# Kernel tuning notes

Hardware: AMD Instinct MI355X
Metric: run time of the kernel (lower is better)

The kernel has to match this reference:

```python
import jax, jax.numpy as jnp
import numpy as np

B, N, M, D = 64, 512, 1024, 128

def setup_inputs() -> dict:
    key = jax.random.key(0)
    ks = jax.random.split(key, 7)
    s = 1.0 / np.sqrt(D)
    return {
        "h_c": jax.random.normal(ks[0], (B, N, D), dtype=jnp.float32),
        "h_p": jax.random.normal(ks[1], (B, M, D), dtype=jnp.float32),
        "U_w": jax.random.normal(ks[2], (D, D), dtype=jnp.float32) * s,
        "U_b": jax.random.normal(ks[3], (D,), dtype=jnp.float32) * s,
        "V_w": jax.random.normal(ks[4], (D, D), dtype=jnp.float32) * s,
        "V_b": jax.random.normal(ks[5], (D,), dtype=jnp.float32) * s,
        "q": jax.random.normal(ks[6], (D,), dtype=jnp.float32),
    }

def reference(h_c, h_p, U_w, U_b, V_w, V_b, q):
    # ReLU-activated linear projections (torch Linear: x @ W.T + b)
    Uc = jax.nn.relu(jnp.einsum('bnd,ed->bne', h_c, U_w) + U_b)  # (B,N,D)
    Vp = jax.nn.relu(jnp.einsum('bmd,ed->bme', h_p, V_w) + V_b)  # (B,M,D)
    # bilinear attention scores and softmax over protein axis
    attn = jnp.einsum('bnd,bmd->bnm', Uc, Vp)                    # (B,N,M)
    weights = jax.nn.softmax(attn, axis=-1)
    context = jnp.einsum('bnm,bmd->bnd', weights, Vp)            # (B,N,D)
    joint = (Uc + context) * q                                   # (B,N,D)
    return joint.mean(axis=1)                                    # (B,D)
```

## Files before the change

kernel.cpp:

```cpp
#include <hip/hip_runtime.h>
#include <hip/hip_bf16.h>
#include <cstdint>

#define BB 64
#define NN 512
#define MM 1024
#define DD 128

typedef __bf16 bf16x8 __attribute__((ext_vector_type(8)));
typedef float f32x4 __attribute__((ext_vector_type(4)));

static __device__ __forceinline__ unsigned short f2bf(float f) {
    union { float f; unsigned int i; } v; v.f = f;
    unsigned int x = v.i;
    x += 0x7FFFu + ((x >> 16) & 1u);
    return (unsigned short)(x >> 16);
}
static __device__ __forceinline__ unsigned int f2bf2(float a, float b) {
    union { __hip_bfloat162 h; unsigned int u; } c;
    c.h = __float22bfloat162_rn(make_float2(a, b));
    return c.u;
}
static __device__ __forceinline__ void async16(const void* g, void* l) {
    __builtin_amdgcn_global_load_lds(
        (const __attribute__((address_space(1))) void*)g,
        (__attribute__((address_space(3))) void*)l, 16, 0, 0);
}

__global__ __launch_bounds__(256) void wcvt_kernel(
    const float* __restrict__ Wu, const float* __restrict__ Wv,
    unsigned short* __restrict__ out)
{
    const float* W = blockIdx.x ? Wv : Wu;
    unsigned short* o = out + blockIdx.x * 16384;
    const float s = blockIdx.x ? 1.0f : 1.44269504088896f;
    #pragma unroll
    for (int i = 0; i < 8; ++i) {
        int ch = i * 256 + threadIdx.x;
        int r = ch >> 4, c = ch & 15;
        const float4* src = (const float4*)(W + r * 128 + c * 8);
        float4 a = src[0], b = src[1];
        uint4 v = { f2bf2(a.x * s, a.y * s), f2bf2(a.z * s, a.w * s),
                    f2bf2(b.x * s, b.y * s), f2bf2(b.z * s, b.w * s) };
        *(uint4*)&o[r * 128 + ((c ^ (r & 7)) << 3)] = v;
    }
}

__global__ __launch_bounds__(256, 4) void proj_kernel(
    const float* __restrict__ hp,
    const float* __restrict__ hc,
    const unsigned short* __restrict__ Wcv,
    const float* __restrict__ Ub,
    const float* __restrict__ Vb,
    unsigned short* __restrict__ Y,
    unsigned short* __restrict__ YT,
    unsigned short* __restrict__ Ucg,
    float* __restrict__ colsum)
{
    __shared__ __align__(16) unsigned short Ws[17408];
    unsigned short* Ys = Ws;
    unsigned short* Ts = Ws + 8192;
    const int t = threadIdx.x;
    const int lane = t & 63;
    const int wave = t >> 6;
    const int n16 = lane & 15, q = lane >> 4;
    const bool isC = blockIdx.x >= (BB * MM / 64);
    const float LOG2E = 1.44269504088896f;

    const long row0 = isC ? (long)(blockIdx.x - BB * MM / 64) * 64
                          : (long)blockIdx.x * 64;
    const float* X = isC ? hc : hp;
    const unsigned short* Wb = isC ? Wcv : (Wcv + 16384);
    const float* bias = isC ? Ub : Vb;

    float4 xv[8];
    {
        const float* xrow = X + (row0 + wave * 16 + n16) * DD + q * 8;
        #pragma unroll
        for (int kk = 0; kk < 4; ++kk) {
            xv[2 * kk]     = *(const float4*)(xrow + kk * 32);
            xv[2 * kk + 1] = *(const float4*)(xrow + kk * 32 + 4);
        }
    }
    #pragma unroll
    for (int i = 0; i < 8; ++i)
        async16(Wb + (wave * 512 + i * 64 + lane) * 8, Ws + wave * 4096 + i * 512);
    __syncthreads();

    f32x4 acc[8];
    #pragma unroll
    for (int j = 0; j < 8; ++j) acc[j] = {0.f, 0.f, 0.f, 0.f};

    #pragma unroll
    for (int kk = 0; kk < 4; ++kk) {
        float4 x0 = xv[2 * kk], x1 = xv[2 * kk + 1];
        union { bf16x8 v; unsigned int u[4]; } a;
        a.u[0] = f2bf2(x0.x, x0.y); a.u[1] = f2bf2(x0.z, x0.w);
        a.u[2] = f2bf2(x1.x, x1.y); a.u[3] = f2bf2(x1.z, x1.w);
        #pragma unroll
        for (int j = 0; j < 8; ++j) {
            bf16x8 b = *(const bf16x8*)&Ws[(j * 16 + n16) * 128
                                           + (((q + 4 * kk) ^ (n16 & 7)) << 3)];
            acc[j] = __builtin_amdgcn_mfma_f32_16x16x32_bf16(a.v, b, acc[j], 0, 0, 0);
        }
    }

    unsigned short yb[8][4];
    float colp[8];
    #pragma unroll
    for (int j = 0; j < 8; ++j) {
        const float bv = isC ? bias[j * 16 + n16] * LOG2E : bias[j * 16 + n16];
        float y[4], s = 0.f;
        #pragma unroll
        for (int r = 0; r < 4; ++r) {
            float v = acc[j][r] + bv;
            v = v > 0.f ? v : 0.f;
            y[r] = v;
            s += v;
        }
        colp[j] = s;
        uint2 u = { f2bf2(y[0], y[1]), f2bf2(y[2], y[3]) };
        *(uint2*)&yb[j][0] = u;
    }
    __syncthreads();

    if (!isC) {
        #pragma unroll
        for (int j = 0; j < 8; ++j) {
            const int e = j * 16 + n16;
            #pragma unroll
            for (int r = 0; r < 4; ++r)
                Ys[(wave * 16 + q * 4 + r) * 128 + e] = yb[j][r];
            *(uint2*)&Ts[e * 72 + wave * 16 + q * 4] = *(uint2*)&yb[j][0];
        }
        __syncthreads();
        uint4* dstY = (uint4*)(Y + row0 * DD);
        const long b = row0 >> 10;
        const long mt = (row0 & 1023) >> 6;
        uint4* dstT = (uint4*)(YT + ((b * 16 + mt) * 128) * 64);
        #pragma unroll
        for (int i = 0; i < 4; ++i) {
            int idx = i * 256 + t;
            dstY[idx] = ((const uint4*)Ys)[idx];
            int e = idx >> 3, m = (idx & 7) * 8;
            dstT[idx] = *(const uint4*)&Ts[e * 72 + m];
        }
    } else {
        #pragma unroll
        for (int j = 0; j < 8; ++j) {
            colp[j] += __shfl_xor(colp[j], 16);
            colp[j] += __shfl_xor(colp[j], 32);
        }
        float* cs = (float*)Ts;
        if (q == 0) {
            #pragma unroll
            for (int j = 0; j < 8; ++j)
                cs[wave * 128 + j * 16 + n16] = colp[j];
        }
        #pragma unroll
        for (int j = 0; j < 8; ++j) {
            const int e = j * 16 + n16;
            #pragma unroll
            for (int r = 0; r < 4; ++r)
                Ys[(wave * 16 + q * 4 + r) * 128 + e] = yb[j][r];
        }
        __syncthreads();
        const int c = (int)(row0 >> 6);
        uint4* dstU = (uint4*)(Ucg + row0 * DD);
        #pragma unroll
        for (int i = 0; i < 4; ++i) {
            int idx = i * 256 + t;
            dstU[idx] = ((const uint4*)Ys)[idx];
        }
        if (t < 128)
            colsum[(long)c * DD + t] = cs[t] + cs[128 + t] + cs[256 + t] + cs[384 + t];
    }
}

static __device__ __forceinline__ void attn_iter(
    int mt, unsigned short* bD, const unsigned short* bR, unsigned short* Ps,
    const unsigned short* __restrict__ vpb,
    const unsigned short* __restrict__ vtb,
    int wave, int lane, int n16, int q, int a_off,
    const bf16x8 (&Bg)[4][4],
    bf16x8 (&aC)[4], bf16x8 (&aN)[4],
    f32x4 (&O)[8], float (&lpart)[4])
{
    const int nx = (mt + 1 > 15) ? 15 : mt + 1;
    {
        const unsigned short* st = vtb + nx * 8192;
        unsigned short* dst = bD + wave * 2048;
        #pragma unroll
        for (int i = 0; i < 4; ++i) {
            int L = wave * 256 + i * 64 + lane;
            int r = L >> 3, sc = L & 7, c = sc ^ (r & 7);
            async16(st + r * 64 + c * 8, dst + i * 512);
        }
    }
    __builtin_amdgcn_sched_barrier(0);
    {
        const unsigned short* pa = vpb + nx * 8192 + a_off;
        #pragma unroll
        for (int kk = 0; kk < 4; ++kk)
            aN[kk] = *(const bf16x8*)(pa + kk * 32);
    }

    f32x4 S[4];
    #pragma unroll
    for (int j = 0; j < 4; ++j) S[j] = {0.f, 0.f, 0.f, 0.f};
    __builtin_amdgcn_s_setprio(1);
    #pragma unroll
    for (int kk = 0; kk < 4; ++kk) {
        #pragma unroll
        for (int j = 0; j < 4; ++j)
            S[j] = __builtin_amdgcn_mfma_f32_16x16x32_bf16(aC[kk], Bg[j][kk], S[j], 0, 0, 0);
    }
    __builtin_amdgcn_s_setprio(0);

    #pragma unroll
    for (int j = 0; j < 4; ++j) {
        float p0 = __builtin_exp2f(S[j][0]);
        float p1 = __builtin_exp2f(S[j][1]);
        float p2 = __builtin_exp2f(S[j][2]);
        float p3 = __builtin_exp2f(S[j][3]);
        lpart[j] += (p0 + p1) + (p2 + p3);
        uint2 u = { f2bf2(p0, p1), f2bf2(p2, p3) };
        *(uint2*)&Ps[(j * 16 + n16) * 72 + wave * 16 + q * 4] = u;
    }
    asm volatile("s_waitcnt vmcnt(8) lgkmcnt(0)" ::: "memory");
    __builtin_amdgcn_s_barrier();
    __builtin_amdgcn_sched_barrier(0);

    __builtin_amdgcn_s_setprio(1);
    #pragma unroll
    for (int kk = 0; kk < 2; ++kk) {
        bf16x8 a = *(const bf16x8*)&Ps[(wave * 16 + n16) * 72 + kk * 32 + q * 8];
        #pragma unroll
        for (int j = 0; j < 8; ++j) {
            bf16x8 bb = *(const bf16x8*)&bR[(j * 16 + n16) * 64 + ((kk * 4 + q) ^ (n16 & 7)) * 8];
            O[j] = __builtin_amdgcn_mfma_f32_16x16x32_bf16(a, bb, O[j], 0, 0, 0);
        }
    }
    __builtin_amdgcn_s_setprio(0);
}

__global__ __launch_bounds__(256, 2) void attn_kernel(
    const unsigned short* __restrict__ Ucg,
    const unsigned short* __restrict__ Vp,
    const unsigned short* __restrict__ VpT,
    float* __restrict__ part)
{
    __shared__ __align__(16) unsigned short smem[33792];
    unsigned short* Ps0 = smem + 24576;
    unsigned short* Ps1 = smem + 29184;

    const int t = threadIdx.x;
    const int lane = t & 63;
    const int wave = t >> 6;
    const int n16 = lane & 15, q = lane >> 4;

    const int id = blockIdx.x;
    const int xcd = id & 7;
    const int slot = id >> 3;
    const int b = xcd * 8 + (slot >> 3);
    const int nt = slot & 7;

    const unsigned short* vpb = Vp + (long)b * MM * DD;
    const unsigned short* vtb = VpT + (long)b * MM * DD;
    const unsigned short* ucb = Ucg + ((long)b * NN + nt * 64) * DD;

    bf16x8 Bg[4][4];
    #pragma unroll
    for (int j = 0; j < 4; ++j)
        #pragma unroll
        for (int kk = 0; kk < 4; ++kk)
            Bg[j][kk] = *(const bf16x8*)&ucb[(j * 16 + n16) * 128 + kk * 32 + q * 8];

    const int a_off = (wave * 16 + n16) * 128 + q * 8;
    bf16x8 aA[4], aB[4];
    #pragma unroll
    for (int kk = 0; kk < 4; ++kk)
        aA[kk] = *(const bf16x8*)&vpb[a_off + kk * 32];
    {
        unsigned short* dst = smem + wave * 2048;
        #pragma unroll
        for (int i = 0; i < 4; ++i) {
            int L = wave * 256 + i * 64 + lane;
            int r = L >> 3, sc = L & 7, c = sc ^ (r & 7);
            async16(vtb + r * 64 + c * 8, dst + i * 512);
        }
    }
    asm volatile("s_waitcnt vmcnt(0) lgkmcnt(0)" ::: "memory");
    __builtin_amdgcn_s_barrier();
    __builtin_amdgcn_sched_barrier(0);

    f32x4 O[8];
    #pragma unroll
    for (int j = 0; j < 8; ++j) O[j] = {0.f, 0.f, 0.f, 0.f};
    float lpart[4] = {0.f, 0.f, 0.f, 0.f};

    unsigned short* bR = smem;
    unsigned short* bD = smem + 8192;
    unsigned short* bT = smem + 16384;
    #pragma unroll 1
    for (int mt = 0; mt < 16; mt += 2) {
        attn_iter(mt, bD, bR, Ps0, vpb, vtb, wave, lane, n16, q, a_off, Bg, aA, aB, O, lpart);
        unsigned short* tp = bR; bR = bD; bD = bT; bT = tp;
        attn_iter(mt + 1, bD, bR, Ps1, vpb, vtb, wave, lane, n16, q, a_off, Bg, aB, aA, O, lpart);
        tp = bR; bR = bD; bD = bT; bT = tp;
    }

    #pragma unroll
    for (int j = 0; j < 4; ++j) {
        lpart[j] += __shfl_xor(lpart[j], 16);
        lpart[j] += __shfl_xor(lpart[j], 32);
    }
    float* lred = (float*)Ps0;
    float* red  = lred + 256;
    if (q == 0) {
        #pragma unroll
        for (int j = 0; j < 4; ++j)
            lred[wave * 64 + j * 16 + n16] = lpart[j];
    }
    __syncthreads();

    float inv[4];
    #pragma unroll
    for (int r = 0; r < 4; ++r) {
        int n = wave * 16 + q * 4 + r;
        inv[r] = 1.0f / (lred[n] + lred[64 + n] + lred[128 + n] + lred[192 + n]);
    }

    #pragma unroll
    for (int j = 0; j < 8; ++j) {
        float s = O[j][0] * inv[0] + O[j][1] * inv[1]
                + O[j][2] * inv[2] + O[j][3] * inv[3];
        s += __shfl_xor(s, 16);
        s += __shfl_xor(s, 32);
        if (q == 0)
            red[wave * 128 + j * 16 + n16] = s;
    }
    __syncthreads();
    if (t < 128) {
        float tot = red[t] + red[128 + t] + red[256 + t] + red[384 + t];
        part[(long)(b * 8 + nt) * DD + t] = tot;
    }
}

__global__ __launch_bounds__(256) void finalize_kernel(
    const float* __restrict__ part, const float* __restrict__ colsum,
    const float* __restrict__ qv, float* __restrict__ out)
{
    int i = blockIdx.x * 256 + threadIdx.x;
    int b = i >> 7, d = i & 127;
    const float* p  = part   + (long)b * 8 * DD + d;
    const float* cs = colsum + (long)b * 8 * DD + d;
    float s = 0.f, u = 0.f;
    #pragma unroll
    for (int nt = 0; nt < 8; ++nt) { s += p[nt * DD]; u += cs[nt * DD]; }
    out[i] = (s + u * 0.69314718055994531f) * qv[d] * (1.0f / (float)NN);
}

extern "C" void kernel_launch(void* const* d_in, const int* in_sizes, int n_in,
                              void* d_out, int out_size, void* d_ws, size_t ws_size,
                              hipStream_t stream) {
    const float* h_c = (const float*)d_in[0];
    const float* h_p = (const float*)d_in[1];
    const float* U_w = (const float*)d_in[2];
    const float* U_b = (const float*)d_in[3];
    const float* V_w = (const float*)d_in[4];
    const float* V_b = (const float*)d_in[5];
    const float* qv  = (const float*)d_in[6];
    float* out = (float*)d_out;

    unsigned short* Vp  = (unsigned short*)d_ws;
    unsigned short* VpT = Vp + (size_t)BB * MM * DD;
    unsigned short* Ucg = VpT + (size_t)BB * MM * DD;
    float* part   = (float*)(Ucg + (size_t)BB * NN * DD);
    float* colsum = part + (size_t)BB * 8 * DD;
    unsigned short* Wcv = (unsigned short*)(colsum + (size_t)BB * 8 * DD);

    wcvt_kernel<<<2, 256, 0, stream>>>(U_w, V_w, Wcv);
    proj_kernel<<<BB * MM / 64 + BB * NN / 64, 256, 0, stream>>>(
        h_p, h_c, Wcv, U_b, V_b, Vp, VpT, Ucg, colsum);
    attn_kernel<<<512, 256, 0, stream>>>(Ucg, Vp, VpT, part);
    finalize_kernel<<<32, 256, 0, stream>>>(part, colsum, qv, out);
}
```

Measured before the change: 141.7 us.

## Fuse weight conversion into projection and software-pipeline attention score computation

The separate weight-to-bf16 conversion kernel is removed. Each projection block now loads the fp32 weights, scales and converts them itself, and stores them into a padded (stride 136) LDS layout in place of the XOR swizzle. In the attention kernel the loop is restructured so that scores and exp for tile mt+1 are computed while the PV matmul of tile mt runs. This uses double-buffered P tiles, a two-tile-ahead V^T prefetch and a prologue that handles the first tile. Dropping the kernel launch saves launch overhead, but every projection block now redoes the weight conversion and loads twice as many bytes of weights.

```diff
diff --git a/kernel.cpp b/kernel.cpp
--- a/kernel.cpp
+++ b/kernel.cpp
@@ -27,29 +27,11 @@
         (__attribute__((address_space(3))) void*)l, 16, 0, 0);
 }
 
-__global__ __launch_bounds__(256) void wcvt_kernel(
-    const float* __restrict__ Wu, const float* __restrict__ Wv,
-    unsigned short* __restrict__ out)
-{
-    const float* W = blockIdx.x ? Wv : Wu;
-    unsigned short* o = out + blockIdx.x * 16384;
-    const float s = blockIdx.x ? 1.0f : 1.44269504088896f;
-    #pragma unroll
-    for (int i = 0; i < 8; ++i) {
-        int ch = i * 256 + threadIdx.x;
-        int r = ch >> 4, c = ch & 15;
-        const float4* src = (const float4*)(W + r * 128 + c * 8);
-        float4 a = src[0], b = src[1];
-        uint4 v = { f2bf2(a.x * s, a.y * s), f2bf2(a.z * s, a.w * s),
-                    f2bf2(b.x * s, b.y * s), f2bf2(b.z * s, b.w * s) };
-        *(uint4*)&o[r * 128 + ((c ^ (r & 7)) << 3)] = v;
-    }
-}
-
 __global__ __launch_bounds__(256, 4) void proj_kernel(
     const float* __restrict__ hp,
     const float* __restrict__ hc,
-    const unsigned short* __restrict__ Wcv,
+    const float* __restrict__ Wu,
+    const float* __restrict__ Wv,
     const float* __restrict__ Ub,
     const float* __restrict__ Vb,
     unsigned short* __restrict__ Y,
@@ -57,7 +39,7 @@
     unsigned short* __restrict__ Ucg,
     float* __restrict__ colsum)
 {
-    __shared__ __align__(16) unsigned short Ws[17408];
+    __shared__ __align__(16) unsigned short Ws[128 * 136];
     unsigned short* Ys = Ws;
     unsigned short* Ts = Ws + 8192;
     const int t = threadIdx.x;
@@ -65,12 +47,12 @@
     const int wave = t >> 6;
     const int n16 = lane & 15, q = lane >> 4;
     const bool isC = blockIdx.x >= (BB * MM / 64);
-    const float LOG2E = 1.44269504088896f;
+    const float ws = isC ? 1.44269504088896f : 1.0f;
 
     const long row0 = isC ? (long)(blockIdx.x - BB * MM / 64) * 64
                           : (long)blockIdx.x * 64;
     const float* X = isC ? hc : hp;
-    const unsigned short* Wb = isC ? Wcv : (Wcv + 16384);
+    const float* Wf = isC ? Wu : Wv;
     const float* bias = isC ? Ub : Vb;
 
     float4 xv[8];
@@ -82,9 +64,17 @@
             xv[2 * kk + 1] = *(const float4*)(xrow + kk * 32 + 4);
         }
     }
-    #pragma unroll
-    for (int i = 0; i < 8; ++i)
-        async16(Wb + (wave * 512 + i * 64 + lane) * 8, Ws + wave * 4096 + i * 512);
+    {
+        const float4* Wg = (const float4*)Wf;
+        #pragma unroll
+        for (int i = 0; i < 16; ++i) {
+            int idx = i * 256 + t;
+            float4 v = Wg[idx];
+            int off = idx * 4;
+            uint2 u = { f2bf2(v.x * ws, v.y * ws), f2bf2(v.z * ws, v.w * ws) };
+            *(uint2*)&Ws[(off >> 7) * 136 + (off & 127)] = u;
+        }
+    }
     __syncthreads();
 
     f32x4 acc[8];
@@ -99,8 +89,7 @@
         a.u[2] = f2bf2(x1.x, x1.y); a.u[3] = f2bf2(x1.z, x1.w);
         #pragma unroll
         for (int j = 0; j < 8; ++j) {
-            bf16x8 b = *(const bf16x8*)&Ws[(j * 16 + n16) * 128
-                                           + (((q + 4 * kk) ^ (n16 & 7)) << 3)];
+            bf16x8 b = *(const bf16x8*)&Ws[(j * 16 + n16) * 136 + q * 8 + kk * 32];
             acc[j] = __builtin_amdgcn_mfma_f32_16x16x32_bf16(a.v, b, acc[j], 0, 0, 0);
         }
     }
@@ -109,7 +98,7 @@
     float colp[8];
     #pragma unroll
     for (int j = 0; j < 8; ++j) {
-        const float bv = isC ? bias[j * 16 + n16] * LOG2E : bias[j * 16 + n16];
+        const float bv = bias[j * 16 + n16] * ws;
         float y[4], s = 0.f;
         #pragma unroll
         for (int r = 0; r < 4; ++r) {
@@ -178,7 +167,8 @@
 }
 
 static __device__ __forceinline__ void attn_iter(
-    int mt, unsigned short* bD, const unsigned short* bR, unsigned short* Ps,
+    int mt, unsigned short* bD, const unsigned short* bR,
+    unsigned short* PsW, const unsigned short* PsR,
     const unsigned short* __restrict__ vpb,
     const unsigned short* __restrict__ vtb,
     int wave, int lane, int n16, int q, int a_off,
@@ -186,7 +176,7 @@
     bf16x8 (&aC)[4], bf16x8 (&aN)[4],
     f32x4 (&O)[8], float (&lpart)[4])
 {
-    const int nx = (mt + 1 > 15) ? 15 : mt + 1;
+    const int nx = (mt + 2 > 15) ? 15 : mt + 2;
     {
         const unsigned short* st = vtb + nx * 8192;
         unsigned short* dst = bD + wave * 2048;
@@ -204,37 +194,37 @@
         for (int kk = 0; kk < 4; ++kk)
             aN[kk] = *(const bf16x8*)(pa + kk * 32);
     }
-
-    f32x4 S[4];
-    #pragma unroll
-    for (int j = 0; j < 4; ++j) S[j] = {0.f, 0.f, 0.f, 0.f};
+    asm volatile("s_waitcnt vmcnt(8)" ::: "memory");
+    __builtin_amdgcn_sched_barrier(0);
+
+    if (mt < 15) {
+        f32x4 S[4];
+        #pragma unroll
+        for (int j = 0; j < 4; ++j) S[j] = {0.f, 0.f, 0.f, 0.f};
+        __builtin_amdgcn_s_setprio(1);
+        #pragma unroll
+        for (int kk = 0; kk < 4; ++kk) {
+            #pragma unroll
+            for (int j = 0; j < 4; ++j)
+                S[j] = __builtin_amdgcn_mfma_f32_16x16x32_bf16(aC[kk], Bg[j][kk], S[j], 0, 0, 0);
+        }
+        __builtin_amdgcn_s_setprio(0);
+        #pragma unroll
+        for (int j = 0; j < 4; ++j) {
+            float p0 = __builtin_exp2f(S[j][0]);
+            float p1 = __builtin_exp2f(S[j][1]);
+            float p2 = __builtin_exp2f(S[j][2]);
+            float p3 = __builtin_exp2f(S[j][3]);
+            lpart[j] += (p0 + p1) + (p2 + p3);
+            uint2 u = { f2bf2(p0, p1), f2bf2(p2, p3) };
+            *(uint2*)&PsW[(j * 16 + n16) * 72 + wave * 16 + q * 4] = u;
+        }
+    }
+
     __builtin_amdgcn_s_setprio(1);
     #pragma unroll
-    for (int kk = 0; kk < 4; ++kk) {
-        #pragma unroll
-        for (int j = 0; j < 4; ++j)
-            S[j] = __builtin_amdgcn_mfma_f32_16x16x32_bf16(aC[kk], Bg[j][kk], S[j], 0, 0, 0);
-    }
-    __builtin_amdgcn_s_setprio(0);
-
-    #pragma unroll
-    for (int j = 0; j < 4; ++j) {
-        float p0 = __builtin_exp2f(S[j][0]);
-        float p1 = __builtin_exp2f(S[j][1]);
-        float p2 = __builtin_exp2f(S[j][2]);
-        float p3 = __builtin_exp2f(S[j][3]);
-        lpart[j] += (p0 + p1) + (p2 + p3);
-        uint2 u = { f2bf2(p0, p1), f2bf2(p2, p3) };
-        *(uint2*)&Ps[(j * 16 + n16) * 72 + wave * 16 + q * 4] = u;
-    }
-    asm volatile("s_waitcnt vmcnt(8) lgkmcnt(0)" ::: "memory");
-    __builtin_amdgcn_s_barrier();
-    __builtin_amdgcn_sched_barrier(0);
-
-    __builtin_amdgcn_s_setprio(1);
-    #pragma unroll
     for (int kk = 0; kk < 2; ++kk) {
-        bf16x8 a = *(const bf16x8*)&Ps[(wave * 16 + n16) * 72 + kk * 32 + q * 8];
+        bf16x8 a = *(const bf16x8*)&PsR[(wave * 16 + n16) * 72 + kk * 32 + q * 8];
         #pragma unroll
         for (int j = 0; j < 8; ++j) {
             bf16x8 bb = *(const bf16x8*)&bR[(j * 16 + n16) * 64 + ((kk * 4 + q) ^ (n16 & 7)) * 8];
@@ -242,6 +232,9 @@
         }
     }
     __builtin_amdgcn_s_setprio(0);
+    asm volatile("s_waitcnt lgkmcnt(0)" ::: "memory");
+    __builtin_amdgcn_s_barrier();
+    __builtin_amdgcn_sched_barrier(0);
 }
 
 __global__ __launch_bounds__(256, 2) void attn_kernel(
@@ -281,33 +274,59 @@
     #pragma unroll
     for (int kk = 0; kk < 4; ++kk)
         aA[kk] = *(const bf16x8*)&vpb[a_off + kk * 32];
-    {
-        unsigned short* dst = smem + wave * 2048;
+    #pragma unroll
+    for (int tt = 0; tt < 2; ++tt) {
+        const unsigned short* st = vtb + tt * 8192;
+        unsigned short* dst = smem + tt * 8192 + wave * 2048;
         #pragma unroll
         for (int i = 0; i < 4; ++i) {
             int L = wave * 256 + i * 64 + lane;
             int r = L >> 3, sc = L & 7, c = sc ^ (r & 7);
-            async16(vtb + r * 64 + c * 8, dst + i * 512);
-        }
-    }
-    asm volatile("s_waitcnt vmcnt(0) lgkmcnt(0)" ::: "memory");
+            async16(st + r * 64 + c * 8, dst + i * 512);
+        }
+    }
+    #pragma unroll
+    for (int kk = 0; kk < 4; ++kk)
+        aB[kk] = *(const bf16x8*)&vpb[8192 + a_off + kk * 32];
+
+    float lpart[4] = {0.f, 0.f, 0.f, 0.f};
+    {
+        f32x4 S[4];
+        #pragma unroll
+        for (int j = 0; j < 4; ++j) S[j] = {0.f, 0.f, 0.f, 0.f};
+        #pragma unroll
+        for (int kk = 0; kk < 4; ++kk) {
+            #pragma unroll
+            for (int j = 0; j < 4; ++j)
+                S[j] = __builtin_amdgcn_mfma_f32_16x16x32_bf16(aA[kk], Bg[j][kk], S[j], 0, 0, 0);
+        }
+        #pragma unroll
+        for (int j = 0; j < 4; ++j) {
+            float p0 = __builtin_exp2f(S[j][0]);
+            float p1 = __builtin_exp2f(S[j][1]);
+            float p2 = __builtin_exp2f(S[j][2]);
+            float p3 = __builtin_exp2f(S[j][3]);
+            lpart[j] += (p0 + p1) + (p2 + p3);
+            uint2 u = { f2bf2(p0, p1), f2bf2(p2, p3) };
+            *(uint2*)&Ps0[(j * 16 + n16) * 72 + wave * 16 + q * 4] = u;
+        }
+    }
+    asm volatile("s_waitcnt lgkmcnt(0)" ::: "memory");
     __builtin_amdgcn_s_barrier();
     __builtin_amdgcn_sched_barrier(0);
 
     f32x4 O[8];
     #pragma unroll
     for (int j = 0; j < 8; ++j) O[j] = {0.f, 0.f, 0.f, 0.f};
-    float lpart[4] = {0.f, 0.f, 0.f, 0.f};
-
-    unsigned short* bR = smem;
-    unsigned short* bD = smem + 8192;
-    unsigned short* bT = smem + 16384;
+
+    unsigned short* b0 = smem;
+    unsigned short* b1 = smem + 8192;
+    unsigned short* b2 = smem + 16384;
     #pragma unroll 1
     for (int mt = 0; mt < 16; mt += 2) {
-        attn_iter(mt, bD, bR, Ps0, vpb, vtb, wave, lane, n16, q, a_off, Bg, aA, aB, O, lpart);
-        unsigned short* tp = bR; bR = bD; bD = bT; bT = tp;
-        attn_iter(mt + 1, bD, bR, Ps1, vpb, vtb, wave, lane, n16, q, a_off, Bg, aB, aA, O, lpart);
-        tp = bR; bR = bD; bD = bT; bT = tp;
+        attn_iter(mt,     b2, b0, Ps1, Ps0, vpb, vtb, wave, lane, n16, q, a_off, Bg, aB, aA, O, lpart);
+        attn_iter(mt + 1, b0, b1, Ps0, Ps1, vpb, vtb, wave, lane, n16, q, a_off, Bg, aA, aB, O, lpart);
+        unsigned short* tp = b0; b0 = b2; b2 = b1; b1 = tp;
     }
 
     #pragma unroll
@@ -378,11 +397,9 @@
     unsigned short* Ucg = VpT + (size_t)BB * MM * DD;
     float* part   = (float*)(Ucg + (size_t)BB * NN * DD);
     float* colsum = part + (size_t)BB * 8 * DD;
-    unsigned short* Wcv = (unsigned short*)(colsum + (size_t)BB * 8 * DD);
-
-    wcvt_kernel<<<2, 256, 0, stream>>>(U_w, V_w, Wcv);
+
     proj_kernel<<<BB * MM / 64 + BB * NN / 64, 256, 0, stream>>>(
-        h_p, h_c, Wcv, U_b, V_b, Vp, VpT, Ucg, colsum);
+        h_p, h_c, U_w, V_w, U_b, V_b, Vp, VpT, Ucg, colsum);
     attn_kernel<<<512, 256, 0, stream>>>(Ucg, Vp, VpT, part);
     finalize_kernel<<<32, 256, 0, stream>>>(part, colsum, qv, out);
 }
```

Result: no change. 139.0 us (-1.9%).
